# Kernel tuning notes

Hardware: AMD Instinct MI355X
Metric: run time of the kernel (lower is better)

## Reference

```python
import jax, jax.numpy as jnp
import numpy as np
from jax import lax


def _conv2d(x, w, b, pad):
    out = lax.conv_general_dilated(x, w, window_strides=(1, 1),
                                   padding=[(pad, pad), (pad, pad)])
    return out + b[None, :, None, None]


def _modulated_deform_conv(x, off_w, off_b, w, b, k, pad):
    """Modulated deformable conv (deformable_groups=1, stride=1, 'same' pad)."""
    B, C, H, W = x.shape
    K2 = k * k
    # offset/mask conv: 3*K2 channels -> (dy, dx, mask_logits)
    om = _conv2d(x, off_w, off_b, pad)              # [B, 3*K2, H, W]
    dy, dx, mlog = om[:, :K2], om[:, K2:2 * K2], om[:, 2 * K2:]
    mask = jax.nn.sigmoid(mlog)                     # [B, K2, H, W]

    xp = jnp.pad(x, ((0, 0), (0, 0), (pad, pad), (pad, pad)))
    Hp, Wp = H + 2 * pad, W + 2 * pad
    Ho, Wo = H, W                                   # stride 1, pad = k//2

    ky, kx = jnp.meshgrid(jnp.arange(k), jnp.arange(k), indexing='ij')
    ky = ky.reshape(1, K2, 1, 1).astype(x.dtype)
    kx = kx.reshape(1, K2, 1, 1).astype(x.dtype)
    iy = jnp.arange(Ho, dtype=x.dtype).reshape(1, 1, Ho, 1)
    ix = jnp.arange(Wo, dtype=x.dtype).reshape(1, 1, 1, Wo)

    py = iy + ky + dy                               # [B, K2, Ho, Wo] sample y (padded coords)
    px = ix + kx + dx                               # [B, K2, Ho, Wo] sample x

    y0f = jnp.floor(py); x0f = jnp.floor(px)
    ty = py - y0f; tx = px - x0f
    y0 = y0f.astype(jnp.int32); x0 = x0f.astype(jnp.int32)
    y1 = y0 + 1; x1 = x0 + 1

    xp_flat = xp.reshape(B, C, Hp * Wp)

    def gather(yi, xi):
        valid = ((yi >= 0) & (yi < Hp) & (xi >= 0) & (xi < Wp)).astype(x.dtype)
        yc = jnp.clip(yi, 0, Hp - 1)
        xc = jnp.clip(xi, 0, Wp - 1)
        idx = (yc * Wp + xc).reshape(B, 1, K2 * Ho * Wo)
        v = jnp.take_along_axis(xp_flat, idx, axis=2).reshape(B, C, K2, Ho, Wo)
        return v * valid[:, None]                   # zero-pad outside

    w00 = ((1 - ty) * (1 - tx))[:, None]
    w01 = ((1 - ty) * tx)[:, None]
    w10 = (ty * (1 - tx))[:, None]
    w11 = (ty * tx)[:, None]

    cols = (gather(y0, x0) * w00 + gather(y0, x1) * w01 +
            gather(y1, x0) * w10 + gather(y1, x1) * w11)
    cols = cols * mask[:, None]                     # [B, C, K2, Ho, Wo]

    O = w.shape[0]
    out = jnp.einsum('bckhw,ock->bohw', cols, w.reshape(O, C, K2))
    return out + b[None, :, None, None]


def setup_inputs() -> dict:
    key = jax.random.key(0)
    ks = jax.random.split(key, 12)
    B, Cin, H, W = 8, 64, 56, 56
    Ch = 128  # out_channels // 2

    def rn(k, shape, scale):
        return jax.random.normal(k, shape, dtype=jnp.float32) * scale

    return {
        'x': rn(ks[0], (B, Cin, H, W), 1.0),
        'w3': rn(ks[1], (Ch, Cin, 3, 3), 0.05),
        'b3': rn(ks[2], (Ch,), 0.05),
        'off3_w': rn(ks[3], (3 * 9, Cin, 3, 3), 0.01),
        'off3_b': rn(ks[4], (3 * 9,), 0.01),
        'w5': rn(ks[5], (Ch, Cin, 5, 5), 0.03),
        'b5': rn(ks[6], (Ch,), 0.05),
        'off5_w': rn(ks[7], (3 * 25, Cin, 5, 5), 0.01),
        'off5_b': rn(ks[8], (3 * 25,), 0.01),
        'sub_w': rn(ks[9], (Ch, Cin, 1, 1), 0.1),
        'sub_b': rn(ks[10], (Ch,), 0.05),
    }


def reference(x, w3, b3, off3_w, off3_b, w5, b5, off5_w, off5_b, sub_w, sub_b):
    x3 = _modulated_deform_conv(x, off3_w, off3_b, w3, b3, k=3, pad=1)
    x5 = _modulated_deform_conv(x, off5_w, off5_b, w5, b5, k=5, pad=2)
    xs = _conv2d(x, sub_w, sub_b, pad=0)            # 1x1 shortcut projection
    x3 = x3 + xs
    x5 = x5 + xs
    out = jnp.concatenate((x3, x5), axis=1)
    return jax.nn.relu(out)
```

## Files before the change

### kernel.cpp

```cpp
#include <hip/hip_runtime.h>
#include <hip/hip_bf16.h>
#include <math.h>

typedef __attribute__((ext_vector_type(8))) short short8;
typedef __attribute__((ext_vector_type(4))) float f32x4;

#define US_XP    0
#define N_XP     (8*60*60*64)
#define US_WOFF  (US_XP + N_XP)
#define N_WOFF   (25*2*8*64*8)
#define US_W5    (US_WOFF + N_WOFF)
#define N_W5     (26*2*8*64*8)
#define US_W3    (US_W5 + N_W5)
#define N_W3     (10*2*8*64*8)
#define US_TOT   (US_W3 + N_W3)
#define FB_BYTES (((US_TOT*2) + 15) & ~15)
#define F_BOM    0
#define F_B5     128
#define F_B3     256
#define F_OM     384
#define N_OM     (8*128*3136)
#define N_ITEMS  (8*34*3136)
#define F_OFFS   (F_OM + N_OM)
#define F_WTS    (F_OFFS + N_ITEMS*4)

__device__ __forceinline__ unsigned short f2bf(float f) {
    union { float f; unsigned u; } v; v.f = f;
    unsigned r = v.u + 0x7FFFu + ((v.u >> 16) & 1u);
    return (unsigned short)(r >> 16);
}
__device__ __forceinline__ unsigned pack2(float lo, float hi) {
    __hip_bfloat162 h = __float22bfloat162_rn(make_float2(lo, hi));
    return *(unsigned*)&h;
}
__device__ __forceinline__ unsigned blend2(unsigned a, unsigned b, unsigned c, unsigned d,
                                           float w00, float w01, float w10, float w11) {
    float lo = __uint_as_float(a << 16) * w00 + __uint_as_float(b << 16) * w01
             + __uint_as_float(c << 16) * w10 + __uint_as_float(d << 16) * w11;
    float hi = __uint_as_float(a & 0xffff0000u) * w00 + __uint_as_float(b & 0xffff0000u) * w01
             + __uint_as_float(c & 0xffff0000u) * w10 + __uint_as_float(d & 0xffff0000u) * w11;
    return pack2(lo, hi);
}

__global__ __launch_bounds__(256) void prep_kernel(
    const float* __restrict__ x,
    const float* __restrict__ w3, const float* __restrict__ b3,
    const float* __restrict__ off3w, const float* __restrict__ off3b,
    const float* __restrict__ w5, const float* __restrict__ b5,
    const float* __restrict__ off5w, const float* __restrict__ off5b,
    const float* __restrict__ subw, const float* __restrict__ subb,
    unsigned short* __restrict__ us, float* __restrict__ fb)
{
    const int NTOT = US_TOT + 384;
    for (int i = blockIdx.x*256 + threadIdx.x; i < NTOT; i += gridDim.x*256) {
        if (i < US_TOT) {
            float v = 0.f;
            if (i < US_WOFF) {
                int c = i & 63, t = i >> 6;
                int xx = t % 60; t /= 60;
                int yy = t % 60; int b = t / 60;
                int y = yy - 2, xc = xx - 2;
                if ((unsigned)y < 56u && (unsigned)xc < 56u)
                    v = x[((b*64 + c)*56 + y)*56 + xc];
            } else {
                int j, mode;
                if (i < US_W5)      { j = i - US_WOFF; mode = 0; }
                else if (i < US_W3) { j = i - US_W5;   mode = 1; }
                else                { j = i - US_W3;   mode = 2; }
                int j8   = j & 7;
                int lane = (j >> 3) & 63;
                int oct  = (j >> 9) & 7;
                int kt   = (j >> 12) & 1;
                int tap  = j >> 13;
                int oc   = oct*16 + (lane & 15);
                int c    = kt*32 + (lane >> 4)*8 + j8;
                if (mode == 0) {
                    if (oc < 27) {
                        int ky = tap/5, kx = tap%5;
                        if (ky>=1 && ky<=3 && kx>=1 && kx<=3)
                            v = off3w[((oc*64 + c)*3 + (ky-1))*3 + (kx-1)];
                    } else if (oc < 102) {
                        v = off5w[((oc-27)*64 + c)*25 + tap];
                    }
                } else if (mode == 1) {
                    v = (tap < 25) ? w5[(oc*64 + c)*25 + tap] : subw[oc*64 + c];
                } else {
                    v = (tap < 9) ? w3[(oc*64 + c)*9 + tap] : subw[oc*64 + c];
                }
            }
            us[i] = f2bf(v);
        } else {
            int fj = i - US_TOT;
            float v;
            if (fj < 128)      v = (fj < 27) ? off3b[fj] : ((fj < 102) ? off5b[fj-27] : 0.f);
            else if (fj < 256) { int o = fj-128; v = b5[o] + subb[o]; }
            else               { int o = fj-256; v = b3[o] + subb[o]; }
            fb[fj] = v;
        }
    }
}

__global__ __launch_bounds__(256) void meta_kernel(
    const float* __restrict__ om, int4* __restrict__ offs, uint2* __restrict__ wts)
{
    const int idx = blockIdx.x*256 + threadIdx.x;
    const int pix = idx % 3136;
    const int r   = idx / 3136;
    const int t   = r % 34;
    const int b   = r / 34;
    int ky, kx, cdy, cdx, cml, HP, SH;
    if (t < 25) { ky = t/5;  kx = t%5;  cdy = 27+t; cdx = 52+t; cml = 77+t; HP = 60; SH = 0; }
    else { int tt = t-25; ky = tt/3; kx = tt%3; cdy = tt; cdx = 9+tt; cml = 18+tt; HP = 58; SH = 1; }
    const int oy = pix/56, ox = pix - oy*56;
    const size_t base = (size_t)b*128*3136 + pix;
    const float dy = om[base + (size_t)cdy*3136];
    const float dx = om[base + (size_t)cdx*3136];
    const float ml = om[base + (size_t)cml*3136];
    const float mask = 1.f / (1.f + __expf(-ml));
    const float py = (float)(oy + ky) + dy;
    const float qx = (float)(ox + kx) + dx;
    const float y0f = floorf(py), x0f = floorf(qx);
    const float ty = py - y0f, tx = qx - x0f;
    const int y0 = (int)y0f, x0 = (int)x0f, y1 = y0+1, x1 = x0+1;
    float w00 = (1.f-ty)*(1.f-tx)*mask;
    float w01 = (1.f-ty)*tx*mask;
    float w10 = ty*(1.f-tx)*mask;
    float w11 = ty*tx*mask;
    const bool vy0 = (unsigned)y0 < (unsigned)HP, vy1 = (unsigned)y1 < (unsigned)HP;
    const bool vx0 = (unsigned)x0 < (unsigned)HP, vx1 = (unsigned)x1 < (unsigned)HP;
    if (!(vy0 && vx0)) w00 = 0.f;
    if (!(vy0 && vx1)) w01 = 0.f;
    if (!(vy1 && vx0)) w10 = 0.f;
    if (!(vy1 && vx1)) w11 = 0.f;
    const int yc0 = min(max(y0,0),HP-1)+SH, yc1 = min(max(y1,0),HP-1)+SH;
    const int xc0 = min(max(x0,0),HP-1)+SH, xc1 = min(max(x1,0),HP-1)+SH;
    offs[idx] = make_int4((yc0*60+xc0)<<7, (yc0*60+xc1)<<7, (yc1*60+xc0)<<7, (yc1*60+xc1)<<7);
    wts[idx]  = make_uint2(pack2(w00,w01), pack2(w10,w11));
}

template<int PXT, bool DEFORM>
__global__ __launch_bounds__(256, 3) void convm(
    const unsigned short* __restrict__ xp,
    const int4* __restrict__ offs, const uint2* __restrict__ wts,
    float* __restrict__ out,
    const unsigned short* __restrict__ wpA, const float* __restrict__ biasA,
    const unsigned short* __restrict__ wpB, const float* __restrict__ biasB,
    int ntA, int ntB, int k2A, int k2B, int tofsA, int tofsB,
    int outc0A, int outc0B, int out_cs)
{
    const int kind  = DEFORM ? (int)(blockIdx.x & 1) : 0;
    const int pxblk = DEFORM ? (int)(blockIdx.x >> 1) : (int)blockIdx.x;
    const unsigned short* wp = kind ? wpB : wpA;
    const float* bias = kind ? biasB : biasA;
    const int ntaps = kind ? ntB : ntA;
    const int K2    = kind ? k2B : k2A;
    const int tofs  = kind ? tofsB : tofsA;
    const int outc0 = kind ? outc0B : outc0A;

    const int b    = blockIdx.y;
    const int pix0 = pxblk * PXT;
    const int lane = threadIdx.x & 63;
    const int wave = threadIdx.x >> 6;
    const int r15 = lane & 15, q4 = lane >> 4;
    const int cg  = lane & 7,  pr = lane >> 3;

    constexpr int NIT = PXT / 32;
    constexpr int NPT = PXT / 16;

    __shared__ unsigned short cols[2][PXT*72];

    f32x4 acc[2][NPT];
#pragma unroll
    for (int i = 0; i < 2; ++i)
#pragma unroll
        for (int pt = 0; pt < NPT; ++pt) acc[i][pt] = (f32x4){0.f,0.f,0.f,0.f};

    const unsigned short* xpb = xp + (size_t)b*(60*60*64);
    const char* xb = (const char*)xpb;

    int coff[NIT], mbase[NIT];
#pragma unroll
    for (int it = 0; it < NIT; ++it) {
        const int px  = wave*(NIT*8) + it*8 + pr;
        const int pix = pix0 + px;
        const int oy  = pix/56, ox = pix - oy*56;
        coff[it]  = (((oy+2)*60) + ox + 2) << 7;
        mbase[it] = (b*34 + tofs)*3136 + pix;
    }

    auto stage = [&](int tap, unsigned short* buf) {
        int koff = 0;
        if (!DEFORM) { int ky = tap/5, kx = tap - ky*5; koff = ((ky-2)*60 + (kx-2)) << 7; }
#pragma unroll
        for (int it = 0; it < NIT; ++it) {
            const int px = wave*(NIT*8) + it*8 + pr;
            uint4 res;
            if (!DEFORM) {
                res = *(const uint4*)(xb + coff[it] + koff + cg*16);
            } else if (tap >= K2) {
                res = *(const uint4*)(xb + coff[it] + cg*16);
            } else {
                const int mi = mbase[it] + tap*3136;
                const int4 o4 = offs[mi];
                const uint2 wq = wts[mi];
                const float w00 = __uint_as_float(wq.x << 16);
                const float w01 = __uint_as_float(wq.x & 0xffff0000u);
                const float w10 = __uint_as_float(wq.y << 16);
                const float w11 = __uint_as_float(wq.y & 0xffff0000u);
                const uint4 qa = *(const uint4*)(xb + o4.x + cg*16);
                const uint4 qb = *(const uint4*)(xb + o4.y + cg*16);
                const uint4 qc = *(const uint4*)(xb + o4.z + cg*16);
                const uint4 qd = *(const uint4*)(xb + o4.w + cg*16);
                res.x = blend2(qa.x, qb.x, qc.x, qd.x, w00, w01, w10, w11);
                res.y = blend2(qa.y, qb.y, qc.y, qd.y, w00, w01, w10, w11);
                res.z = blend2(qa.z, qb.z, qc.z, qd.z, w00, w01, w10, w11);
                res.w = blend2(qa.w, qb.w, qc.w, qd.w, w00, w01, w10, w11);
            }
            *(uint4*)&buf[px*72 + cg*8] = res;
        }
    };

    auto gemm = [&](int tap, const unsigned short* buf) {
#pragma unroll
        for (int kt = 0; kt < 2; ++kt) {
            short8 Af[2];
#pragma unroll
            for (int i = 0; i < 2; ++i)
                Af[i] = *(const short8*)(wp + ((size_t)((tap*2+kt)*8 + wave*2 + i)*64 + lane)*8);
#pragma unroll
            for (int pt = 0; pt < NPT; ++pt) {
                short8 Bf = *(const short8*)(buf + (pt*16 + r15)*72 + kt*32 + q4*8);
#pragma unroll
                for (int i = 0; i < 2; ++i)
                    acc[i][pt] = __builtin_amdgcn_mfma_f32_16x16x32_bf16(Af[i], Bf, acc[i][pt], 0, 0, 0);
            }
        }
    };

    stage(0, cols[0]);
    __syncthreads();
    for (int t = 0; t < ntaps; ++t) {
        if (t + 1 < ntaps) stage(t + 1, cols[(t+1) & 1]);
        gemm(t, cols[t & 1]);
        __syncthreads();
    }

#pragma unroll
    for (int i = 0; i < 2; ++i)
#pragma unroll
    for (int pt = 0; pt < NPT; ++pt)
#pragma unroll
    for (int reg = 0; reg < 4; ++reg) {
        const int oc  = (wave*2 + i)*16 + q4*4 + reg;
        const int pix = pix0 + pt*16 + r15;
        float v = acc[i][pt][reg] + bias[oc];
        if (DEFORM) v = fmaxf(v, 0.f);
        out[((size_t)b*out_cs + outc0 + oc)*3136 + pix] = v;
    }
}

extern "C" void kernel_launch(void* const* d_in, const int* in_sizes, int n_in,
                              void* d_out, int out_size, void* d_ws, size_t ws_size,
                              hipStream_t stream)
{
    (void)in_sizes; (void)n_in; (void)out_size; (void)ws_size;
    const float* x     = (const float*)d_in[0];
    const float* w3    = (const float*)d_in[1];
    const float* b3    = (const float*)d_in[2];
    const float* off3w = (const float*)d_in[3];
    const float* off3b = (const float*)d_in[4];
    const float* w5    = (const float*)d_in[5];
    const float* b5    = (const float*)d_in[6];
    const float* off5w = (const float*)d_in[7];
    const float* off5b = (const float*)d_in[8];
    const float* subw  = (const float*)d_in[9];
    const float* subb  = (const float*)d_in[10];

    unsigned short* us = (unsigned short*)d_ws;
    float* fb   = (float*)((char*)d_ws + FB_BYTES);
    float* omb  = fb + F_OM;
    int4*  offs = (int4*)(fb + F_OFFS);
    uint2* wts  = (uint2*)(fb + F_WTS);
    float* out  = (float*)d_out;

    prep_kernel<<<dim3(1024), dim3(256), 0, stream>>>(
        x, w3, b3, off3w, off3b, w5, b5, off5w, off5b, subw, subb, us, fb);

    convm<32, false><<<dim3(98, 8), dim3(256), 0, stream>>>(
        us + US_XP, nullptr, nullptr, omb,
        us + US_WOFF, fb + F_BOM, us + US_WOFF, fb + F_BOM,
        25, 25, 25, 25, 0, 0, 0, 0, 128);

    meta_kernel<<<dim3(N_ITEMS/256), dim3(256), 0, stream>>>(omb, offs, wts);

    convm<64, true><<<dim3(98, 8), dim3(256), 0, stream>>>(
        us + US_XP, offs, wts, out,
        us + US_W5, fb + F_B5, us + US_W3, fb + F_B3,
        26, 10, 25, 9, 0, 25, 128, 0, 256);
}
```

Before: 190.9 us.

## Software-pipeline deformable gather loads and drop LDS staging in offset conv

The offset/mask convolution becomes a dedicated kernel that reads its B operands straight from global memory into MFMA, with no LDS staging or barriers, and declares a higher occupancy bound. The deformable conv kernel now prefetches offset and weight metadata two taps ahead and issues the corner gathers one tap ahead into registers, then blends and writes to LDS after the GEMM. This hides gather latency behind MFMA work. The cost is higher register pressure, which may reduce occupancy.

```diff
diff --git a/kernel.cpp b/kernel.cpp
--- a/kernel.cpp
+++ b/kernel.cpp
@@ -138,88 +138,166 @@
     wts[idx]  = make_uint2(pack2(w00,w01), pack2(w10,w11));
 }
 
-template<int PXT, bool DEFORM>
-__global__ __launch_bounds__(256, 3) void convm(
+__global__ __launch_bounds__(256, 6) void convo(
+    const unsigned short* __restrict__ xp, float* __restrict__ om,
+    const unsigned short* __restrict__ wp, const float* __restrict__ bias)
+{
+    const int b    = blockIdx.y;
+    const int pix0 = blockIdx.x * 32;
+    const int lane = threadIdx.x & 63;
+    const int wave = threadIdx.x >> 6;
+    const int r15 = lane & 15, q4 = lane >> 4;
+
+    const char* xb = (const char*)(xp + (size_t)b*(60*60*64));
+
+    int bofs[2];
+#pragma unroll
+    for (int pt = 0; pt < 2; ++pt) {
+        const int pix = pix0 + pt*16 + r15;
+        const int oy = pix/56, ox = pix - oy*56;
+        bofs[pt] = ((oy+2)*60 + ox + 2)*128 + q4*16;
+    }
+
+    f32x4 acc[2][2] = {{{0.f,0.f,0.f,0.f},{0.f,0.f,0.f,0.f}},
+                       {{0.f,0.f,0.f,0.f},{0.f,0.f,0.f,0.f}}};
+
+#pragma unroll 5
+    for (int t = 0; t < 25; ++t) {
+        const int ky = t/5, kx = t - ky*5;
+        const int koff = ((ky-2)*60 + (kx-2)) * 128;
+#pragma unroll
+        for (int kt = 0; kt < 2; ++kt) {
+            short8 A0 = *(const short8*)(wp + (size_t)((t*2+kt)*8 + wave*2    )*512 + lane*8);
+            short8 A1 = *(const short8*)(wp + (size_t)((t*2+kt)*8 + wave*2 + 1)*512 + lane*8);
+#pragma unroll
+            for (int pt = 0; pt < 2; ++pt) {
+                short8 B = *(const short8*)(xb + bofs[pt] + koff + kt*64);
+                acc[0][pt] = __builtin_amdgcn_mfma_f32_16x16x32_bf16(A0, B, acc[0][pt], 0, 0, 0);
+                acc[1][pt] = __builtin_amdgcn_mfma_f32_16x16x32_bf16(A1, B, acc[1][pt], 0, 0, 0);
+            }
+        }
+    }
+#pragma unroll
+    for (int i = 0; i < 2; ++i)
+#pragma unroll
+    for (int pt = 0; pt < 2; ++pt)
+#pragma unroll
+    for (int reg = 0; reg < 4; ++reg) {
+        const int oc  = (wave*2 + i)*16 + q4*4 + reg;
+        const int pix = pix0 + pt*16 + r15;
+        om[((size_t)b*128 + oc)*3136 + pix] = acc[i][pt][reg] + bias[oc];
+    }
+}
+
+__global__ __launch_bounds__(256, 3) void convd(
     const unsigned short* __restrict__ xp,
     const int4* __restrict__ offs, const uint2* __restrict__ wts,
     float* __restrict__ out,
-    const unsigned short* __restrict__ wpA, const float* __restrict__ biasA,
-    const unsigned short* __restrict__ wpB, const float* __restrict__ biasB,
-    int ntA, int ntB, int k2A, int k2B, int tofsA, int tofsB,
-    int outc0A, int outc0B, int out_cs)
-{
-    const int kind  = DEFORM ? (int)(blockIdx.x & 1) : 0;
-    const int pxblk = DEFORM ? (int)(blockIdx.x >> 1) : (int)blockIdx.x;
-    const unsigned short* wp = kind ? wpB : wpA;
-    const float* bias = kind ? biasB : biasA;
-    const int ntaps = kind ? ntB : ntA;
-    const int K2    = kind ? k2B : k2A;
-    const int tofs  = kind ? tofsB : tofsA;
-    const int outc0 = kind ? outc0B : outc0A;
+    const unsigned short* __restrict__ wp5, const float* __restrict__ bias5,
+    const unsigned short* __restrict__ wp3, const float* __restrict__ bias3)
+{
+    const int kind  = blockIdx.x & 1;
+    const int pxblk = blockIdx.x >> 1;
+    const unsigned short* wp = kind ? wp3 : wp5;
+    const float* bias = kind ? bias3 : bias5;
+    const int ntaps = kind ? 10 : 26;
+    const int K2    = kind ? 9  : 25;
+    const int tofs  = kind ? 25 : 0;
+    const int outc0 = kind ? 0  : 128;
 
     const int b    = blockIdx.y;
-    const int pix0 = pxblk * PXT;
+    const int pix0 = pxblk * 64;
     const int lane = threadIdx.x & 63;
     const int wave = threadIdx.x >> 6;
     const int r15 = lane & 15, q4 = lane >> 4;
     const int cg  = lane & 7,  pr = lane >> 3;
 
-    constexpr int NIT = PXT / 32;
-    constexpr int NPT = PXT / 16;
-
-    __shared__ unsigned short cols[2][PXT*72];
-
-    f32x4 acc[2][NPT];
+    __shared__ unsigned short cols[2][64*72];
+
+    f32x4 acc[2][4];
 #pragma unroll
     for (int i = 0; i < 2; ++i)
 #pragma unroll
-        for (int pt = 0; pt < NPT; ++pt) acc[i][pt] = (f32x4){0.f,0.f,0.f,0.f};
-
-    const unsigned short* xpb = xp + (size_t)b*(60*60*64);
-    const char* xb = (const char*)xpb;
-
-    int coff[NIT], mbase[NIT];
-#pragma unroll
-    for (int it = 0; it < NIT; ++it) {
-        const int px  = wave*(NIT*8) + it*8 + pr;
+        for (int pt = 0; pt < 4; ++pt) acc[i][pt] = (f32x4){0.f,0.f,0.f,0.f};
+
+    const char* xb = (const char*)(xp + (size_t)b*(60*60*64));
+
+    int coff[2], mbase[2];
+#pragma unroll
+    for (int it = 0; it < 2; ++it) {
+        const int px  = wave*16 + it*8 + pr;
         const int pix = pix0 + px;
         const int oy  = pix/56, ox = pix - oy*56;
         coff[it]  = (((oy+2)*60) + ox + 2) << 7;
         mbase[it] = (b*34 + tofs)*3136 + pix;
     }
 
-    auto stage = [&](int tap, unsigned short* buf) {
-        int koff = 0;
-        if (!DEFORM) { int ky = tap/5, kx = tap - ky*5; koff = ((ky-2)*60 + (kx-2)) << 7; }
-#pragma unroll
-        for (int it = 0; it < NIT; ++it) {
-            const int px = wave*(NIT*8) + it*8 + pr;
+    uint4 C[2][4];
+    uint2 WC[2];
+    int4  MO0[2], MO1[2];
+    uint2 MW0[2], MW1[2];
+
+    auto load_meta0 = [&](int s) {
+        const int sc = min(s, K2-1);
+#pragma unroll
+        for (int it = 0; it < 2; ++it) {
+            const int mi = mbase[it] + sc*3136;
+            MO0[it] = offs[mi]; MW0[it] = wts[mi];
+        }
+    };
+    auto load_meta1 = [&](int s) {
+        const int sc = min(s, K2-1);
+#pragma unroll
+        for (int it = 0; it < 2; ++it) {
+            const int mi = mbase[it] + sc*3136;
+            MO1[it] = offs[mi]; MW1[it] = wts[mi];
+        }
+    };
+    auto issue_corners = [&](int s) {
+        if (s >= K2) {
+#pragma unroll
+            for (int it = 0; it < 2; ++it)
+                C[it][0] = *(const uint4*)(xb + coff[it] + cg*16);
+        } else if (s & 1) {
+#pragma unroll
+            for (int it = 0; it < 2; ++it) {
+                const int4 o4 = MO1[it]; WC[it] = MW1[it];
+                C[it][0] = *(const uint4*)(xb + o4.x + cg*16);
+                C[it][1] = *(const uint4*)(xb + o4.y + cg*16);
+                C[it][2] = *(const uint4*)(xb + o4.z + cg*16);
+                C[it][3] = *(const uint4*)(xb + o4.w + cg*16);
+            }
+        } else {
+#pragma unroll
+            for (int it = 0; it < 2; ++it) {
+                const int4 o4 = MO0[it]; WC[it] = MW0[it];
+                C[it][0] = *(const uint4*)(xb + o4.x + cg*16);
+                C[it][1] = *(const uint4*)(xb + o4.y + cg*16);
+                C[it][2] = *(const uint4*)(xb + o4.z + cg*16);
+                C[it][3] = *(const uint4*)(xb + o4.w + cg*16);
+            }
+        }
+    };
+    auto blend_write = [&](int s, unsigned short* buf) {
+#pragma unroll
+        for (int it = 0; it < 2; ++it) {
+            const int px = wave*16 + it*8 + pr;
             uint4 res;
-            if (!DEFORM) {
-                res = *(const uint4*)(xb + coff[it] + koff + cg*16);
-            } else if (tap >= K2) {
-                res = *(const uint4*)(xb + coff[it] + cg*16);
+            if (s >= K2) {
+                res = C[it][0];
             } else {
-                const int mi = mbase[it] + tap*3136;
-                const int4 o4 = offs[mi];
-                const uint2 wq = wts[mi];
-                const float w00 = __uint_as_float(wq.x << 16);
-                const float w01 = __uint_as_float(wq.x & 0xffff0000u);
-                const float w10 = __uint_as_float(wq.y << 16);
-                const float w11 = __uint_as_float(wq.y & 0xffff0000u);
-                const uint4 qa = *(const uint4*)(xb + o4.x + cg*16);
-                const uint4 qb = *(const uint4*)(xb + o4.y + cg*16);
-                const uint4 qc = *(const uint4*)(xb + o4.z + cg*16);
-                const uint4 qd = *(const uint4*)(xb + o4.w + cg*16);
-                res.x = blend2(qa.x, qb.x, qc.x, qd.x, w00, w01, w10, w11);
-                res.y = blend2(qa.y, qb.y, qc.y, qd.y, w00, w01, w10, w11);
-                res.z = blend2(qa.z, qb.z, qc.z, qd.z, w00, w01, w10, w11);
-                res.w = blend2(qa.w, qb.w, qc.w, qd.w, w00, w01, w10, w11);
+                const float w00 = __uint_as_float(WC[it].x << 16);
+                const float w01 = __uint_as_float(WC[it].x & 0xffff0000u);
+                const float w10 = __uint_as_float(WC[it].y << 16);
+                const float w11 = __uint_as_float(WC[it].y & 0xffff0000u);
+                res.x = blend2(C[it][0].x, C[it][1].x, C[it][2].x, C[it][3].x, w00, w01, w10, w11);
+                res.y = blend2(C[it][0].y, C[it][1].y, C[it][2].y, C[it][3].y, w00, w01, w10, w11);
+                res.z = blend2(C[it][0].z, C[it][1].z, C[it][2].z, C[it][3].z, w00, w01, w10, w11);
+                res.w = blend2(C[it][0].w, C[it][1].w, C[it][2].w, C[it][3].w, w00, w01, w10, w11);
             }
             *(uint4*)&buf[px*72 + cg*8] = res;
         }
     };
-
     auto gemm = [&](int tap, const unsigned short* buf) {
 #pragma unroll
         for (int kt = 0; kt < 2; ++kt) {
@@ -228,7 +306,7 @@
             for (int i = 0; i < 2; ++i)
                 Af[i] = *(const short8*)(wp + ((size_t)((tap*2+kt)*8 + wave*2 + i)*64 + lane)*8);
 #pragma unroll
-            for (int pt = 0; pt < NPT; ++pt) {
+            for (int pt = 0; pt < 4; ++pt) {
                 short8 Bf = *(const short8*)(buf + (pt*16 + r15)*72 + kt*32 + q4*8);
 #pragma unroll
                 for (int i = 0; i < 2; ++i)
@@ -237,25 +315,38 @@
         }
     };
 
-    stage(0, cols[0]);
+    load_meta0(0);
+    load_meta1(1);
+    issue_corners(0);
+    load_meta0(2);
+    blend_write(0, cols[0]);
+    issue_corners(1);
+    load_meta1(3);
     __syncthreads();
+
     for (int t = 0; t < ntaps; ++t) {
-        if (t + 1 < ntaps) stage(t + 1, cols[(t+1) & 1]);
         gemm(t, cols[t & 1]);
+        if (t + 1 < ntaps) {
+            blend_write(t + 1, cols[(t+1) & 1]);
+            if (t + 2 < ntaps) {
+                issue_corners(t + 2);
+                if ((t & 1) == 0) load_meta0(t + 4);
+                else              load_meta1(t + 4);
+            }
+        }
         __syncthreads();
     }
 
 #pragma unroll
     for (int i = 0; i < 2; ++i)
 #pragma unroll
-    for (int pt = 0; pt < NPT; ++pt)
+    for (int pt = 0; pt < 4; ++pt)
 #pragma unroll
     for (int reg = 0; reg < 4; ++reg) {
         const int oc  = (wave*2 + i)*16 + q4*4 + reg;
         const int pix = pix0 + pt*16 + r15;
-        float v = acc[i][pt][reg] + bias[oc];
-        if (DEFORM) v = fmaxf(v, 0.f);
-        out[((size_t)b*out_cs + outc0 + oc)*3136 + pix] = v;
+        float v = fmaxf(acc[i][pt][reg] + bias[oc], 0.f);
+        out[((size_t)b*256 + outc0 + oc)*3136 + pix] = v;
     }
 }
 
@@ -286,15 +377,12 @@
     prep_kernel<<<dim3(1024), dim3(256), 0, stream>>>(
         x, w3, b3, off3w, off3b, w5, b5, off5w, off5b, subw, subb, us, fb);
 
-    convm<32, false><<<dim3(98, 8), dim3(256), 0, stream>>>(
-        us + US_XP, nullptr, nullptr, omb,
-        us + US_WOFF, fb + F_BOM, us + US_WOFF, fb + F_BOM,
-        25, 25, 25, 25, 0, 0, 0, 0, 128);
+    convo<<<dim3(98, 8), dim3(256), 0, stream>>>(
+        us + US_XP, omb, us + US_WOFF, fb + F_BOM);
 
     meta_kernel<<<dim3(N_ITEMS/256), dim3(256), 0, stream>>>(omb, offs, wts);
 
-    convm<64, true><<<dim3(98, 8), dim3(256), 0, stream>>>(
+    convd<<<dim3(98, 8), dim3(256), 0, stream>>>(
         us + US_XP, offs, wts, out,
-        us + US_W5, fb + F_B5, us + US_W3, fb + F_B3,
-        26, 10, 25, 9, 0, 25, 128, 0, 256);
-}
+        us + US_W5, fb + F_B5, us + US_W3, fb + F_B3);
+}
```

Measured after the change: 242.0 us. +26.8%, slower.

## Fuse offset conv with sampling metadata and process two taps per sync

Applied to the files above, without the earlier changes.

The offset/mask convolution kernel and the separate meta kernel are merged. The offset conv result is staged in shared memory and converted straight to gather offsets and bilinear weights, so the fp32 offset map no longer makes a round trip through global memory and one launch is removed. Both conv kernels now use 64-pixel tiles and stage two taps per double-buffer step, which halves the barriers per tap. The offset conv grid shrinks from 98 to 49 pixel blocks, and the offset weights are padded to 26 taps.

```diff
diff --git a/kernel.cpp b/kernel.cpp
--- a/kernel.cpp
+++ b/kernel.cpp
@@ -8,7 +8,7 @@
 #define US_XP    0
 #define N_XP     (8*60*60*64)
 #define US_WOFF  (US_XP + N_XP)
-#define N_WOFF   (25*2*8*64*8)
+#define N_WOFF   (26*2*8*64*8)
 #define US_W5    (US_WOFF + N_WOFF)
 #define N_W5     (26*2*8*64*8)
 #define US_W3    (US_W5 + N_W5)
@@ -18,10 +18,8 @@
 #define F_BOM    0
 #define F_B5     128
 #define F_B3     256
-#define F_OM     384
-#define N_OM     (8*128*3136)
 #define N_ITEMS  (8*34*3136)
-#define F_OFFS   (F_OM + N_OM)
+#define F_OFFS   384
 #define F_WTS    (F_OFFS + N_ITEMS*4)
 
 __device__ __forceinline__ unsigned short f2bf(float f) {
@@ -75,11 +73,11 @@
                 int oc   = oct*16 + (lane & 15);
                 int c    = kt*32 + (lane >> 4)*8 + j8;
                 if (mode == 0) {
-                    if (oc < 27) {
+                    if (oc < 27 && tap < 25) {
                         int ky = tap/5, kx = tap%5;
                         if (ky>=1 && ky<=3 && kx>=1 && kx<=3)
                             v = off3w[((oc*64 + c)*3 + (ky-1))*3 + (kx-1)];
-                    } else if (oc < 102) {
+                    } else if (oc >= 27 && oc < 102 && tap < 25) {
                         v = off5w[((oc-27)*64 + c)*25 + tap];
                     }
                 } else if (mode == 1) {
@@ -100,107 +98,180 @@
     }
 }
 
-__global__ __launch_bounds__(256) void meta_kernel(
-    const float* __restrict__ om, int4* __restrict__ offs, uint2* __restrict__ wts)
+__global__ __launch_bounds__(256, 4) void convo2(
+    const unsigned short* __restrict__ xp,
+    const unsigned short* __restrict__ wp, const float* __restrict__ bias,
+    int4* __restrict__ offs, uint2* __restrict__ wts)
 {
-    const int idx = blockIdx.x*256 + threadIdx.x;
-    const int pix = idx % 3136;
-    const int r   = idx / 3136;
-    const int t   = r % 34;
-    const int b   = r / 34;
-    int ky, kx, cdy, cdx, cml, HP, SH;
-    if (t < 25) { ky = t/5;  kx = t%5;  cdy = 27+t; cdx = 52+t; cml = 77+t; HP = 60; SH = 0; }
-    else { int tt = t-25; ky = tt/3; kx = tt%3; cdy = tt; cdx = 9+tt; cml = 18+tt; HP = 58; SH = 1; }
-    const int oy = pix/56, ox = pix - oy*56;
-    const size_t base = (size_t)b*128*3136 + pix;
-    const float dy = om[base + (size_t)cdy*3136];
-    const float dx = om[base + (size_t)cdx*3136];
-    const float ml = om[base + (size_t)cml*3136];
-    const float mask = 1.f / (1.f + __expf(-ml));
-    const float py = (float)(oy + ky) + dy;
-    const float qx = (float)(ox + kx) + dx;
-    const float y0f = floorf(py), x0f = floorf(qx);
-    const float ty = py - y0f, tx = qx - x0f;
-    const int y0 = (int)y0f, x0 = (int)x0f, y1 = y0+1, x1 = x0+1;
-    float w00 = (1.f-ty)*(1.f-tx)*mask;
-    float w01 = (1.f-ty)*tx*mask;
-    float w10 = ty*(1.f-tx)*mask;
-    float w11 = ty*tx*mask;
-    const bool vy0 = (unsigned)y0 < (unsigned)HP, vy1 = (unsigned)y1 < (unsigned)HP;
-    const bool vx0 = (unsigned)x0 < (unsigned)HP, vx1 = (unsigned)x1 < (unsigned)HP;
-    if (!(vy0 && vx0)) w00 = 0.f;
-    if (!(vy0 && vx1)) w01 = 0.f;
-    if (!(vy1 && vx0)) w10 = 0.f;
-    if (!(vy1 && vx1)) w11 = 0.f;
-    const int yc0 = min(max(y0,0),HP-1)+SH, yc1 = min(max(y1,0),HP-1)+SH;
-    const int xc0 = min(max(x0,0),HP-1)+SH, xc1 = min(max(x1,0),HP-1)+SH;
-    offs[idx] = make_int4((yc0*60+xc0)<<7, (yc0*60+xc1)<<7, (yc1*60+xc0)<<7, (yc1*60+xc1)<<7);
-    wts[idx]  = make_uint2(pack2(w00,w01), pack2(w10,w11));
-}
-
-template<int PXT, bool DEFORM>
-__global__ __launch_bounds__(256, 3) void convm(
-    const unsigned short* __restrict__ xp,
-    const int4* __restrict__ offs, const uint2* __restrict__ wts,
-    float* __restrict__ out,
-    const unsigned short* __restrict__ wpA, const float* __restrict__ biasA,
-    const unsigned short* __restrict__ wpB, const float* __restrict__ biasB,
-    int ntA, int ntB, int k2A, int k2B, int tofsA, int tofsB,
-    int outc0A, int outc0B, int out_cs)
-{
-    const int kind  = DEFORM ? (int)(blockIdx.x & 1) : 0;
-    const int pxblk = DEFORM ? (int)(blockIdx.x >> 1) : (int)blockIdx.x;
-    const unsigned short* wp = kind ? wpB : wpA;
-    const float* bias = kind ? biasB : biasA;
-    const int ntaps = kind ? ntB : ntA;
-    const int K2    = kind ? k2B : k2A;
-    const int tofs  = kind ? tofsB : tofsA;
-    const int outc0 = kind ? outc0B : outc0A;
-
     const int b    = blockIdx.y;
-    const int pix0 = pxblk * PXT;
+    const int pix0 = blockIdx.x * 64;
     const int lane = threadIdx.x & 63;
     const int wave = threadIdx.x >> 6;
     const int r15 = lane & 15, q4 = lane >> 4;
     const int cg  = lane & 7,  pr = lane >> 3;
 
-    constexpr int NIT = PXT / 32;
-    constexpr int NPT = PXT / 16;
-
-    __shared__ unsigned short cols[2][PXT*72];
-
-    f32x4 acc[2][NPT];
+    __shared__ __align__(16) unsigned short cols[2][2][64*72];
+
+    f32x4 acc[2][4];
 #pragma unroll
     for (int i = 0; i < 2; ++i)
 #pragma unroll
-        for (int pt = 0; pt < NPT; ++pt) acc[i][pt] = (f32x4){0.f,0.f,0.f,0.f};
-
-    const unsigned short* xpb = xp + (size_t)b*(60*60*64);
-    const char* xb = (const char*)xpb;
-
-    int coff[NIT], mbase[NIT];
-#pragma unroll
-    for (int it = 0; it < NIT; ++it) {
-        const int px  = wave*(NIT*8) + it*8 + pr;
+        for (int pt = 0; pt < 4; ++pt) acc[i][pt] = (f32x4){0.f,0.f,0.f,0.f};
+
+    const char* xb = (const char*)(xp + (size_t)b*(60*60*64));
+
+    int coff[2];
+#pragma unroll
+    for (int it = 0; it < 2; ++it) {
+        const int px  = wave*16 + it*8 + pr;
+        const int pix = pix0 + px;
+        const int oy  = pix/56, ox = pix - oy*56;
+        coff[it] = (((oy+2)*60) + ox + 2) << 7;
+    }
+
+    auto stage_tap = [&](int t, unsigned short* buf) {
+        int koff = 0;
+        if (t < 25) { int ky = t/5, kx = t - ky*5; koff = ((ky-2)*60 + (kx-2)) << 7; }
+#pragma unroll
+        for (int it = 0; it < 2; ++it) {
+            const int px = wave*16 + it*8 + pr;
+            uint4 res = *(const uint4*)(xb + coff[it] + koff + cg*16);
+            *(uint4*)&buf[px*72 + cg*8] = res;
+        }
+    };
+    auto gemm_tap = [&](int tap, const unsigned short* buf) {
+#pragma unroll
+        for (int kt = 0; kt < 2; ++kt) {
+            short8 Af[2];
+#pragma unroll
+            for (int i = 0; i < 2; ++i)
+                Af[i] = *(const short8*)(wp + ((size_t)((tap*2+kt)*8 + wave*2 + i)*64 + lane)*8);
+#pragma unroll
+            for (int pt = 0; pt < 4; ++pt) {
+                short8 Bf = *(const short8*)(buf + (pt*16 + r15)*72 + kt*32 + q4*8);
+#pragma unroll
+                for (int i = 0; i < 2; ++i)
+                    acc[i][pt] = __builtin_amdgcn_mfma_f32_16x16x32_bf16(Af[i], Bf, acc[i][pt], 0, 0, 0);
+            }
+        }
+    };
+
+    stage_tap(0, cols[0][0]);
+    stage_tap(1, cols[0][1]);
+    __syncthreads();
+    for (int r = 0; r < 13; ++r) {
+        if (r + 1 < 13) {
+            stage_tap(2*r+2, cols[(r+1)&1][0]);
+            stage_tap(2*r+3, cols[(r+1)&1][1]);
+        }
+        gemm_tap(2*r,   cols[r&1][0]);
+        gemm_tap(2*r+1, cols[r&1][1]);
+        __syncthreads();
+    }
+
+    float* omt = (float*)cols;
+#pragma unroll
+    for (int i = 0; i < 2; ++i)
+#pragma unroll
+    for (int pt = 0; pt < 4; ++pt)
+#pragma unroll
+    for (int reg = 0; reg < 4; ++reg) {
+        const int oc = (wave*2 + i)*16 + q4*4 + reg;
+        const int px = pt*16 + r15;
+        omt[oc*64 + px] = acc[i][pt][reg] + bias[oc];
+    }
+    __syncthreads();
+
+    const int tid = threadIdx.x;
+#pragma unroll
+    for (int itr = 0; itr < 9; ++itr) {
+        const int idx = itr*256 + tid;
+        if (idx >= 34*64) break;
+        const int t  = idx >> 6;
+        const int px = idx & 63;
+        const int pix = pix0 + px;
+        const int oy = pix/56, ox = pix - oy*56;
+        int ky, kx, cdy, cdx, cml, HP, SH;
+        if (t < 25) { ky = t/5; kx = t%5; cdy = 27+t; cdx = 52+t; cml = 77+t; HP = 60; SH = 0; }
+        else { int tt = t-25; ky = tt/3; kx = tt%3; cdy = tt; cdx = 9+tt; cml = 18+tt; HP = 58; SH = 1; }
+        const float dy = omt[cdy*64 + px];
+        const float dx = omt[cdx*64 + px];
+        const float ml = omt[cml*64 + px];
+        const float mask = 1.f / (1.f + __expf(-ml));
+        const float py = (float)(oy + ky) + dy;
+        const float qx = (float)(ox + kx) + dx;
+        const float y0f = floorf(py), x0f = floorf(qx);
+        const float ty = py - y0f, tx = qx - x0f;
+        const int y0 = (int)y0f, x0 = (int)x0f, y1 = y0+1, x1 = x0+1;
+        float w00 = (1.f-ty)*(1.f-tx)*mask;
+        float w01 = (1.f-ty)*tx*mask;
+        float w10 = ty*(1.f-tx)*mask;
+        float w11 = ty*tx*mask;
+        const bool vy0 = (unsigned)y0 < (unsigned)HP, vy1 = (unsigned)y1 < (unsigned)HP;
+        const bool vx0 = (unsigned)x0 < (unsigned)HP, vx1 = (unsigned)x1 < (unsigned)HP;
+        if (!(vy0 && vx0)) w00 = 0.f;
+        if (!(vy0 && vx1)) w01 = 0.f;
+        if (!(vy1 && vx0)) w10 = 0.f;
+        if (!(vy1 && vx1)) w11 = 0.f;
+        const int yc0 = min(max(y0,0),HP-1)+SH, yc1 = min(max(y1,0),HP-1)+SH;
+        const int xc0 = min(max(x0,0),HP-1)+SH, xc1 = min(max(x1,0),HP-1)+SH;
+        const int mi = (b*34 + t)*3136 + pix;
+        offs[mi] = make_int4((yc0*60+xc0)<<7, (yc0*60+xc1)<<7, (yc1*60+xc0)<<7, (yc1*60+xc1)<<7);
+        wts[mi]  = make_uint2(pack2(w00,w01), pack2(w10,w11));
+    }
+}
+
+__global__ __launch_bounds__(256, 4) void convd2(
+    const unsigned short* __restrict__ xp,
+    const int4* __restrict__ offs, const uint2* __restrict__ wts,
+    float* __restrict__ out,
+    const unsigned short* __restrict__ wp5, const float* __restrict__ bias5,
+    const unsigned short* __restrict__ wp3, const float* __restrict__ bias3)
+{
+    const int kind  = blockIdx.z;
+    const unsigned short* wp = kind ? wp3 : wp5;
+    const float* bias = kind ? bias3 : bias5;
+    const int R     = kind ? 5  : 13;
+    const int K2    = kind ? 9  : 25;
+    const int tofs  = kind ? 25 : 0;
+    const int outc0 = kind ? 0  : 128;
+
+    const int b    = blockIdx.y;
+    const int pix0 = blockIdx.x * 64;
+    const int lane = threadIdx.x & 63;
+    const int wave = threadIdx.x >> 6;
+    const int r15 = lane & 15, q4 = lane >> 4;
+    const int cg  = lane & 7,  pr = lane >> 3;
+
+    __shared__ __align__(16) unsigned short cols[2][2][64*72];
+
+    f32x4 acc[2][4];
+#pragma unroll
+    for (int i = 0; i < 2; ++i)
+#pragma unroll
+        for (int pt = 0; pt < 4; ++pt) acc[i][pt] = (f32x4){0.f,0.f,0.f,0.f};
+
+    const char* xb = (const char*)(xp + (size_t)b*(60*60*64));
+
+    int coff[2], mbase[2];
+#pragma unroll
+    for (int it = 0; it < 2; ++it) {
+        const int px  = wave*16 + it*8 + pr;
         const int pix = pix0 + px;
         const int oy  = pix/56, ox = pix - oy*56;
         coff[it]  = (((oy+2)*60) + ox + 2) << 7;
         mbase[it] = (b*34 + tofs)*3136 + pix;
     }
 
-    auto stage = [&](int tap, unsigned short* buf) {
-        int koff = 0;
-        if (!DEFORM) { int ky = tap/5, kx = tap - ky*5; koff = ((ky-2)*60 + (kx-2)) << 7; }
-#pragma unroll
-        for (int it = 0; it < NIT; ++it) {
-            const int px = wave*(NIT*8) + it*8 + pr;
+    auto stage_tap = [&](int t, unsigned short* buf) {
+#pragma unroll
+        for (int it = 0; it < 2; ++it) {
+            const int px = wave*16 + it*8 + pr;
             uint4 res;
-            if (!DEFORM) {
-                res = *(const uint4*)(xb + coff[it] + koff + cg*16);
-            } else if (tap >= K2) {
+            if (t >= K2) {
                 res = *(const uint4*)(xb + coff[it] + cg*16);
             } else {
-                const int mi = mbase[it] + tap*3136;
+                const int mi = mbase[it] + t*3136;
                 const int4 o4 = offs[mi];
                 const uint2 wq = wts[mi];
                 const float w00 = __uint_as_float(wq.x << 16);
@@ -219,8 +290,7 @@
             *(uint4*)&buf[px*72 + cg*8] = res;
         }
     };
-
-    auto gemm = [&](int tap, const unsigned short* buf) {
+    auto gemm_tap = [&](int tap, const unsigned short* buf) {
 #pragma unroll
         for (int kt = 0; kt < 2; ++kt) {
             short8 Af[2];
@@ -228,7 +298,7 @@
             for (int i = 0; i < 2; ++i)
                 Af[i] = *(const short8*)(wp + ((size_t)((tap*2+kt)*8 + wave*2 + i)*64 + lane)*8);
 #pragma unroll
-            for (int pt = 0; pt < NPT; ++pt) {
+            for (int pt = 0; pt < 4; ++pt) {
                 short8 Bf = *(const short8*)(buf + (pt*16 + r15)*72 + kt*32 + q4*8);
 #pragma unroll
                 for (int i = 0; i < 2; ++i)
@@ -237,25 +307,29 @@
         }
     };
 
-    stage(0, cols[0]);
+    stage_tap(0, cols[0][0]);
+    stage_tap(1, cols[0][1]);
     __syncthreads();
-    for (int t = 0; t < ntaps; ++t) {
-        if (t + 1 < ntaps) stage(t + 1, cols[(t+1) & 1]);
-        gemm(t, cols[t & 1]);
+    for (int r = 0; r < R; ++r) {
+        if (r + 1 < R) {
+            stage_tap(2*r+2, cols[(r+1)&1][0]);
+            stage_tap(2*r+3, cols[(r+1)&1][1]);
+        }
+        gemm_tap(2*r,   cols[r&1][0]);
+        gemm_tap(2*r+1, cols[r&1][1]);
         __syncthreads();
     }
 
 #pragma unroll
     for (int i = 0; i < 2; ++i)
 #pragma unroll
-    for (int pt = 0; pt < NPT; ++pt)
+    for (int pt = 0; pt < 4; ++pt)
 #pragma unroll
     for (int reg = 0; reg < 4; ++reg) {
         const int oc  = (wave*2 + i)*16 + q4*4 + reg;
         const int pix = pix0 + pt*16 + r15;
-        float v = acc[i][pt][reg] + bias[oc];
-        if (DEFORM) v = fmaxf(v, 0.f);
-        out[((size_t)b*out_cs + outc0 + oc)*3136 + pix] = v;
+        float v = fmaxf(acc[i][pt][reg] + bias[oc], 0.f);
+        out[((size_t)b*256 + outc0 + oc)*3136 + pix] = v;
     }
 }
 
@@ -278,7 +352,6 @@
 
     unsigned short* us = (unsigned short*)d_ws;
     float* fb   = (float*)((char*)d_ws + FB_BYTES);
-    float* omb  = fb + F_OM;
     int4*  offs = (int4*)(fb + F_OFFS);
     uint2* wts  = (uint2*)(fb + F_WTS);
     float* out  = (float*)d_out;
@@ -286,15 +359,10 @@
     prep_kernel<<<dim3(1024), dim3(256), 0, stream>>>(
         x, w3, b3, off3w, off3b, w5, b5, off5w, off5b, subw, subb, us, fb);
 
-    convm<32, false><<<dim3(98, 8), dim3(256), 0, stream>>>(
-        us + US_XP, nullptr, nullptr, omb,
-        us + US_WOFF, fb + F_BOM, us + US_WOFF, fb + F_BOM,
-        25, 25, 25, 25, 0, 0, 0, 0, 128);
-
-    meta_kernel<<<dim3(N_ITEMS/256), dim3(256), 0, stream>>>(omb, offs, wts);
-
-    convm<64, true><<<dim3(98, 8), dim3(256), 0, stream>>>(
+    convo2<<<dim3(49, 8), dim3(256), 0, stream>>>(
+        us + US_XP, us + US_WOFF, fb + F_BOM, offs, wts);
+
+    convd2<<<dim3(49, 8, 2), dim3(256), 0, stream>>>(
         us + US_XP, offs, wts, out,
-        us + US_W5, fb + F_B5, us + US_W3, fb + F_B3,
-        26, 10, 25, 9, 0, 25, 128, 0, 256);
-}
+        us + US_W5, fb + F_B5, us + US_W3, fb + F_B3);
+}
```

After: 173.5 us. 9.1% less time.
